# Kernel tuning notes

Measured on AMD Instinct MI355X. Metric: run time of the kernel, lower is better.

## Reference

```python
import jax, jax.numpy as jnp
import numpy as np

B, Q, K, D, H = 8, 200, 16384, 256, 8
ALIGN_K, CROSS_K, FF = 96, 1024, 1024
DH = D // H

def _l2norm(x):
    n = jnp.linalg.norm(x, axis=-1, keepdims=True)
    return x / jnp.maximum(n, 1e-6)

def _layernorm(x, g, b):
    mu = jnp.mean(x, axis=-1, keepdims=True)
    v = jnp.var(x, axis=-1, keepdims=True)
    return (x - mu) / jnp.sqrt(v + 1e-5) * g + b

def _mha(xq, xk, xv, in_w, in_b, out_w, out_b, bias=None):
    # torch nn.MultiheadAttention (batch_first, eval mode)
    wq, wk, wv = jnp.split(in_w, 3, axis=0)
    bq, bk, bv = jnp.split(in_b, 3, axis=0)
    def heads(x, w, bb):
        y = x @ w.T + bb
        return y.reshape(x.shape[0], x.shape[1], H, DH).transpose(0, 2, 1, 3)
    qh, kh, vh = heads(xq, wq, bq), heads(xk, wk, bk), heads(xv, wv, bv)
    s = jnp.einsum('bhqd,bhkd->bhqk', qh, kh) / (DH ** 0.5)
    if bias is not None:
        s = s + bias
    a = jax.nn.softmax(s, axis=-1)
    o = jnp.einsum('bhqk,bhkd->bhqd', a, vh).transpose(0, 2, 1, 3).reshape(xq.shape[0], xq.shape[1], D)
    return o @ out_w.T + out_b

def setup_inputs():
    key = jax.random.key(0)
    ks = jax.random.split(key, 40)
    r = lambda i, sh, s=1.0: jax.random.normal(ks[i], sh, jnp.float32) * s
    W = 0.02
    return dict(
        q=r(0, (B, Q, D)), q_pos=r(1, (B, Q, D)), memory=r(2, (B, K, D)),
        cross_attn_bias=r(3, (B, Q, K), 0.1),
        align_wq=r(4, (D, D), W), align_wm=r(5, (D, D), W),
        gate_w1=r(6, (D, 2 * D), W), gate_b1=jnp.zeros((D,), jnp.float32),
        gate_w2=r(7, (D, D), W), gate_b2=jnp.zeros((D,), jnp.float32),
        cross_wq=r(8, (D, D), W), cross_wm=r(9, (D, D), W),
        sa_in_w=r(10, (3 * D, D), W), sa_in_b=jnp.zeros((3 * D,), jnp.float32),
        sa_out_w=r(11, (D, D), W), sa_out_b=jnp.zeros((D,), jnp.float32),
        ca_in_w=r(12, (3 * D, D), W), ca_in_b=jnp.zeros((3 * D,), jnp.float32),
        ca_out_w=r(13, (D, D), W), ca_out_b=jnp.zeros((D,), jnp.float32),
        ffn_w1=r(14, (FF, D), W), ffn_b1=jnp.zeros((FF,), jnp.float32),
        ffn_w2=r(15, (D, FF), W), ffn_b2=jnp.zeros((D,), jnp.float32),
        n1_g=jnp.ones((D,), jnp.float32), n1_b=jnp.zeros((D,), jnp.float32),
        n2_g=jnp.ones((D,), jnp.float32), n2_b=jnp.zeros((D,), jnp.float32),
        n3_g=jnp.ones((D,), jnp.float32), n3_b=jnp.zeros((D,), jnp.float32))

def reference(q, q_pos, memory, cross_attn_bias, align_wq, align_wm, gate_w1, gate_b1,
              gate_w2, gate_b2, cross_wq, cross_wm, sa_in_w, sa_in_b, sa_out_w, sa_out_b,
              ca_in_w, ca_in_b, ca_out_w, ca_out_b, ffn_w1, ffn_b1, ffn_w2, ffn_b2,
              n1_g, n1_b, n2_g, n2_b, n3_g, n3_b):
    # --- query-memory align: proj+normalize+sim+topk+gather+softmax+weighted-sum ---
    qn = _l2norm(q @ align_wq.T)
    mn = _l2norm(memory @ align_wm.T)
    sim = jnp.einsum('bqd,bkd->bqk', qn, mn)            # [B,Q,K]
    vals, idx = jax.lax.top_k(sim, ALIGN_K)             # [B,Q,ALIGN_K]
    selected = jax.vmap(lambda m, i: m[i])(memory, idx) # [B,Q,ALIGN_K,D]
    w = jax.nn.softmax(vals, axis=-1)
    aligned = jnp.einsum('bqk,bqkd->bqd', w, selected)
    h = jax.nn.gelu(jnp.concatenate([q, aligned], axis=-1) @ gate_w1.T + gate_b1, approximate=False)
    gate = jax.nn.sigmoid(h @ gate_w2.T + gate_b2)
    qx = q + gate * aligned
    # --- self attention ---
    qk = qx + q_pos
    q2 = _mha(qk, qk, qx, sa_in_w, sa_in_b, sa_out_w, sa_out_b)
    qx = _layernorm(qx + q2, n1_g, n1_b)
    # --- cross-memory sparsify (topk over K) ---
    qn2 = _l2norm(qx @ cross_wq.T)
    mn2 = _l2norm(memory @ cross_wm.T)
    sim2 = jnp.einsum('bqd,bkd->bqk', qn2, mn2)
    importance = sim2.max(axis=1)                       # [B,K]
    _, kidx = jax.lax.top_k(importance, CROSS_K)        # [B,CROSS_K]
    mem_sel = jax.vmap(lambda m, i: m[i])(memory, kidx) # [B,CROSS_K,D]
    bias_sel = jnp.take_along_axis(
        cross_attn_bias, jnp.broadcast_to(kidx[:, None, :], (B, Q, CROSS_K)), axis=2)
    bias4 = jnp.broadcast_to(bias_sel[:, None], (B, H, Q, CROSS_K))
    q2 = _mha(qx + q_pos, mem_sel, mem_sel, ca_in_w, ca_in_b, ca_out_w, ca_out_b, bias4)
    qx = _layernorm(qx + q2, n2_g, n2_b)
    # --- FFN ---
    f = jax.nn.gelu(qx @ ffn_w1.T + ffn_b1, approximate=False) @ ffn_w2.T + ffn_b2
    return _layernorm(qx + f, n3_g, n3_b)
```

## Files before the change

### kernel.cpp

```cpp
#include <hip/hip_runtime.h>
#include <hip/hip_bf16.h>
#include <math.h>

#define B_ 8
#define Q_ 200
#define K_ 16384
#define D_ 256
#define H_ 8
#define DH_ 32
#define ALIGNK_ 96
#define CROSSK_ 1024
#define FF_ 1024
#define BQ_ (B_*Q_)
#define BK_ (B_*K_)

typedef unsigned short u16;
typedef short bf16x8 __attribute__((ext_vector_type(8)));
typedef float f32x4 __attribute__((ext_vector_type(4)));

__device__ __forceinline__ float b2f(u16 u){ return __uint_as_float(((unsigned)u)<<16); }
__device__ __forceinline__ u16 f2b(float f){
  unsigned x = __float_as_uint(f);
  unsigned r = x + 0x7FFFu + ((x>>16)&1u);
  return (u16)(r>>16);
}
__device__ __forceinline__ unsigned p2u(float lo, float hi){
  return (unsigned)f2b(lo) | ((unsigned)f2b(hi)<<16);
}
__device__ __forceinline__ uint4 pk8(float4 a, float4 b){
  return make_uint4(p2u(a.x,a.y), p2u(a.z,a.w), p2u(b.x,b.y), p2u(b.z,b.w));
}
__device__ __forceinline__ unsigned fkey(float f){ unsigned b=__float_as_uint(f); return (b&0x80000000u)? ~b : (b|0x80000000u); }
__device__ __forceinline__ float funkey(unsigned k){ unsigned b=(k&0x80000000u)? (k^0x80000000u) : ~k; return __uint_as_float(b); }
__device__ __forceinline__ float gelu_f(float x){ return 0.5f*x*(1.0f+erff(x*0.70710678118654752f)); }
__device__ __forceinline__ float sigmoid_f(float x){ return 1.0f/(1.0f+__expf(-x)); }

struct GArgs {
  const void* A; const void* B; const float* bias;
  float* Cf; u16* Cb; unsigned* amax;
  const int* gather;
  long lda, ldb, ldc;
  long sA, sB, sC, sAmax, sGather;
  int M, N, K, act;
};

template<int AF32, int BF32>
__global__ __launch_bounds__(256) void gemm_bt(GArgs g)
{
  const int tid = threadIdx.x;
  const int bz = blockIdx.z;
  const int m0 = blockIdx.y*64, n0 = blockIdx.x*64;
  const int lane = tid & 63, wave = tid >> 6;
  const int wr = wave >> 1, wc = wave & 1;
  __shared__ __align__(16) u16 As[64][72];
  __shared__ __align__(16) u16 Bs[64][72];
  f32x4 acc[2][2] = {};

  const int lrow = tid>>2;
  const int lk = (tid&3)*16;
  int ar = m0 + lrow; if (ar > g.M-1) ar = g.M-1;
  if (g.gather) ar = g.gather[(long)bz*g.sGather + ar];
  int br = n0 + lrow; if (br > g.N-1) br = g.N-1;
  long aoff = (long)bz*g.sA + (long)ar*g.lda + lk;
  long boff = (long)bz*g.sB + (long)br*g.ldb + lk;

  const int nk = g.K >> 6;
  for (int kt=0; kt<nk; ++kt){
    uint4 wa0, wa1, wb0, wb1;
    if (AF32){
      const float* p = (const float*)g.A + aoff;
      float4 f0 = *(const float4*)(p+0);
      float4 f1 = *(const float4*)(p+4);
      float4 f2v= *(const float4*)(p+8);
      float4 f3 = *(const float4*)(p+12);
      wa0 = pk8(f0,f1); wa1 = pk8(f2v,f3);
    } else {
      const u16* p = (const u16*)g.A + aoff;
      wa0 = *(const uint4*)p; wa1 = *(const uint4*)(p+8);
    }
    if (BF32){
      const float* p = (const float*)g.B + boff;
      float4 f0 = *(const float4*)(p+0);
      float4 f1 = *(const float4*)(p+4);
      float4 f2v= *(const float4*)(p+8);
      float4 f3 = *(const float4*)(p+12);
      wb0 = pk8(f0,f1); wb1 = pk8(f2v,f3);
    } else {
      const u16* p = (const u16*)g.B + boff;
      wb0 = *(const uint4*)p; wb1 = *(const uint4*)(p+8);
    }
    aoff += 64; boff += 64;
    __syncthreads();
    *(uint4*)&As[lrow][lk]   = wa0; *(uint4*)&As[lrow][lk+8] = wa1;
    *(uint4*)&Bs[lrow][lk]   = wb0; *(uint4*)&Bs[lrow][lk+8] = wb1;
    __syncthreads();
    #pragma unroll
    for (int kk=0; kk<2; ++kk){
      const int ko = kk*32 + (lane>>4)*8;
      bf16x8 af0 = *(const bf16x8*)&As[wr*32      + (lane&15)][ko];
      bf16x8 af1 = *(const bf16x8*)&As[wr*32 + 16 + (lane&15)][ko];
      bf16x8 bf0 = *(const bf16x8*)&Bs[wc*32      + (lane&15)][ko];
      bf16x8 bf1 = *(const bf16x8*)&Bs[wc*32 + 16 + (lane&15)][ko];
      acc[0][0] = __builtin_amdgcn_mfma_f32_16x16x32_bf16(af0, bf0, acc[0][0], 0,0,0);
      acc[0][1] = __builtin_amdgcn_mfma_f32_16x16x32_bf16(af0, bf1, acc[0][1], 0,0,0);
      acc[1][0] = __builtin_amdgcn_mfma_f32_16x16x32_bf16(af1, bf0, acc[1][0], 0,0,0);
      acc[1][1] = __builtin_amdgcn_mfma_f32_16x16x32_bf16(af1, bf1, acc[1][1], 0,0,0);
    }
  }

  if (g.amax){
    #pragma unroll
    for (int j=0;j<2;j++){
      float mx = -3.0e38f;
      #pragma unroll
      for (int i=0;i<2;i++)
        #pragma unroll
        for (int r=0;r<4;r++) mx = fmaxf(mx, acc[i][j][r]);
      mx = fmaxf(mx, __shfl_xor(mx, 16));
      mx = fmaxf(mx, __shfl_xor(mx, 32));
      if ((lane>>4)==0){
        int n = n0 + wc*32 + j*16 + (lane&15);
        if (n < g.N) atomicMax(&g.amax[(long)bz*g.sAmax + n], fkey(mx));
      }
    }
    return;
  }

  #pragma unroll
  for (int i=0;i<2;i++)
  #pragma unroll
  for (int j=0;j<2;j++)
  #pragma unroll
  for (int r=0;r<4;r++){
    int m = m0 + wr*32 + i*16 + (lane>>4)*4 + r;
    int n = n0 + wc*32 + j*16 + (lane&15);
    if (m < g.M && n < g.N){
      float v = acc[i][j][r];
      if (g.bias) v += g.bias[n];
      if (g.act==1) v = gelu_f(v);
      else if (g.act==2) v = sigmoid_f(v);
      long ci = (long)bz*g.sC + (long)m*g.ldc + n;
      if (g.Cf) g.Cf[ci] = v; else g.Cb[ci] = f2b(v);
    }
  }
}

template<int AF32>
__global__ __launch_bounds__(256) void proj_l2norm(
    const void* Ain, long lda, const float* W, u16* outp, int R)
{
  __shared__ __align__(16) u16 As[64][72];
  __shared__ __align__(16) u16 Bs[256][72];
  const int tid = threadIdx.x;
  const int m0 = blockIdx.x*64;
  const int lane = tid & 63, wave = tid >> 6;
  f32x4 acc[16] = {};

  const int lrow = tid>>2, lk = (tid&3)*16;
  int ar = m0 + lrow; if (ar > R-1) ar = R-1;

  for (int kt=0; kt<4; ++kt){
    uint4 wa0, wa1;
    if (AF32){
      const float* p = (const float*)Ain + (long)ar*lda + kt*64 + lk;
      wa0 = pk8(*(const float4*)(p+0), *(const float4*)(p+4));
      wa1 = pk8(*(const float4*)(p+8), *(const float4*)(p+12));
    } else {
      const u16* p = (const u16*)Ain + (long)ar*lda + kt*64 + lk;
      wa0 = *(const uint4*)p; wa1 = *(const uint4*)(p+8);
    }
    uint4 wb[8];
    {
      const float* wp = W + (long)tid*256 + kt*64;
      #pragma unroll
      for (int i=0;i<8;i++)
        wb[i] = pk8(*(const float4*)(wp + i*8), *(const float4*)(wp + i*8 + 4));
    }
    __syncthreads();
    *(uint4*)&As[lrow][lk] = wa0; *(uint4*)&As[lrow][lk+8] = wa1;
    #pragma unroll
    for (int i=0;i<8;i++) *(uint4*)&Bs[tid][i*8] = wb[i];
    __syncthreads();
    #pragma unroll
    for (int kk=0; kk<2; ++kk){
      const int ko = kk*32 + (lane>>4)*8;
      bf16x8 af = *(const bf16x8*)&As[wave*16 + (lane&15)][ko];
      #pragma unroll
      for (int jj=0; jj<16; jj++){
        bf16x8 bfr = *(const bf16x8*)&Bs[jj*16 + (lane&15)][ko];
        acc[jj] = __builtin_amdgcn_mfma_f32_16x16x32_bf16(af, bfr, acc[jj], 0,0,0);
      }
    }
  }

  #pragma unroll
  for (int r=0;r<4;r++){
    float ssq = 0.f;
    #pragma unroll
    for (int jj=0;jj<16;jj++) ssq += acc[jj][r]*acc[jj][r];
    ssq += __shfl_xor(ssq,1); ssq += __shfl_xor(ssq,2);
    ssq += __shfl_xor(ssq,4); ssq += __shfl_xor(ssq,8);
    float inv = 1.0f/fmaxf(sqrtf(ssq), 1e-6f);
    int row = m0 + wave*16 + (lane>>4)*4 + r;
    if (row < R){
      u16* op = outp + (long)row*256 + (lane&15);
      #pragma unroll
      for (int jj=0;jj<16;jj++) op[jj*16] = f2b(acc[jj][r]*inv);
    }
  }
}

__global__ __launch_bounds__(256) void topk_kernel(const float* inF, const unsigned* inK,
    long in_stride, int RANK, float* out_val, int* out_idx)
{
  __shared__ int red[2][4];
  __shared__ int redt[4];
  __shared__ int poss;
  int row = blockIdx.x, tid = threadIdx.x;
  unsigned kr[64];
  if (inF){
    const float4* p = (const float4*)(inF + (long)row*in_stride);
    #pragma unroll
    for (int jj=0;jj<16;jj++){
      float4 v = p[tid + jj*256];
      kr[jj*4+0]=fkey(v.x); kr[jj*4+1]=fkey(v.y); kr[jj*4+2]=fkey(v.z); kr[jj*4+3]=fkey(v.w);
    }
  } else {
    const uint4* p = (const uint4*)(inK + (long)row*in_stride);
    #pragma unroll
    for (int jj=0;jj<16;jj++){
      uint4 v = p[tid + jj*256];
      kr[jj*4+0]=v.x; kr[jj*4+1]=v.y; kr[jj*4+2]=v.z; kr[jj*4+3]=v.w;
    }
  }
  if (tid==0) poss = 0;

  unsigned u = 0; bool exact = false; int pp = 0;
  for (int bit=31; bit>=0; --bit){
    unsigned cand = u | (1u<<bit);
    int c = 0;
    #pragma unroll
    for (int j=0;j<64;j++) c += (kr[j] >= cand) ? 1 : 0;
    #pragma unroll
    for (int off=32; off; off>>=1) c += __shfl_down(c, off);
    if ((tid&63)==0) red[pp][tid>>6] = c;
    __syncthreads();
    c = red[pp][0]+red[pp][1]+red[pp][2]+red[pp][3];
    pp ^= 1;
    if (c >= RANK){
      u = cand;
      if (c == RANK){ exact = true; break; }
    }
  }

  int t = 0;
  if (!exact){
    int cgt = 0;
    #pragma unroll
    for (int j=0;j<64;j++) cgt += (kr[j] > u) ? 1 : 0;
    #pragma unroll
    for (int off=32; off; off>>=1) cgt += __shfl_down(cgt, off);
    __syncthreads();
    if ((tid&63)==0) redt[tid>>6] = cgt;
    __syncthreads();
    cgt = redt[0]+redt[1]+redt[2]+redt[3];
    int Req = RANK - cgt;
    for (int bit=13; bit>=0; --bit){
      int cand = t | (1<<bit);
      int c = 0;
      #pragma unroll
      for (int j=0;j<64;j++){
        int e = (tid<<2) + (j&3) + ((j>>2)<<10);
        c += (kr[j]==u && e < cand) ? 1 : 0;
      }
      #pragma unroll
      for (int off=32; off; off>>=1) c += __shfl_down(c, off);
      __syncthreads();
      if ((tid&63)==0) redt[tid>>6] = c;
      __syncthreads();
      c = redt[0]+redt[1]+redt[2]+redt[3];
      if (c < Req) t = cand;
    }
  }
  __syncthreads();
  #pragma unroll
  for (int j=0;j<64;j++){
    int e = (tid<<2) + (j&3) + ((j>>2)<<10);
    unsigned kk = kr[j];
    bool win = exact ? (kk >= u) : (kk > u || (kk == u && e <= t));
    if (win){
      int p2 = atomicAdd(&poss, 1);
      out_val[(long)row*RANK + p2] = funkey(kk);
      out_idx[(long)row*RANK + p2] = e;
    }
  }
}

__global__ __launch_bounds__(256) void align_combine(const float* vals, const int* idx,
    const float* memory, float* alignedv)
{
  __shared__ float w[96];
  __shared__ int id[96];
  __shared__ float reds[2];
  int row = blockIdx.x, tid = threadIdx.x;
  int b = row / 200;
  if (tid < 96){ w[tid] = vals[(long)row*96 + tid]; id[tid] = idx[(long)row*96 + tid]; }
  __syncthreads();
  if (tid < 64){
    float a = w[tid];
    float bb2 = (tid < 32) ? w[64+tid] : -3e38f;
    float m = fmaxf(a, bb2);
    #pragma unroll
    for (int off=32; off; off>>=1) m = fmaxf(m, __shfl_xor(m, off));
    if (tid==0) reds[0] = m;
  }
  __syncthreads();
  float m = reds[0];
  if (tid < 96) w[tid] = __expf(w[tid]-m);
  __syncthreads();
  if (tid < 64){
    float a = w[tid] + ((tid<32)? w[64+tid] : 0.f);
    #pragma unroll
    for (int off=32; off; off>>=1) a += __shfl_xor(a, off);
    if (tid==0) reds[1] = a;
  }
  __syncthreads();
  float invs = 1.0f/reds[1];
  float acc = 0.f;
  const float* mb = memory + (long)b*K_*D_;
  for (int k=0;k<96;k++) acc += w[k] * mb[(long)id[k]*D_ + tid];
  alignedv[(long)row*256 + tid] = acc*invs;
}

__global__ void make_cat(const float* q, const float* alignedv, u16* cat)
{
  int row = blockIdx.x, tid = threadIdx.x;
  long i = (long)row*256 + tid;
  cat[(long)row*512 + tid]       = f2b(q[i]);
  cat[(long)row*512 + 256 + tid] = f2b(alignedv[i]);
}

__global__ void combine_gate(const float* q, const float* q_pos, const float* alignedv,
    const float* gate, float* qx, u16* qx_b, u16* qk_b)
{
  int row = blockIdx.x, tid = threadIdx.x;
  long i = (long)row*256 + tid;
  float v = q[i] + gate[i]*alignedv[i];
  qx[i] = v;
  qx_b[i] = f2b(v);
  qk_b[i] = f2b(v + q_pos[i]);
}

__global__ __launch_bounds__(256) void add_ln(const float* x, const float* y,
    const float* g, const float* bb, const float* q_pos,
    float* out_f, u16* out_b, u16* out_pos_b)
{
  __shared__ float red[8];
  int row = blockIdx.x, tid = threadIdx.x;
  long i = (long)row*256 + tid;
  float t = fminf(fmaxf(x[i] + y[i], -1e6f), 1e6f);
  float s1 = t, s2 = t*t;
  #pragma unroll
  for (int off=32; off; off>>=1){ s1 += __shfl_down(s1,off); s2 += __shfl_down(s2,off); }
  if ((tid&63)==0){ red[(tid>>6)*2] = s1; red[(tid>>6)*2+1] = s2; }
  __syncthreads();
  s1 = red[0]+red[2]+red[4]+red[6];
  s2 = red[1]+red[3]+red[5]+red[7];
  float mu = s1 * (1.0f/256.0f);
  float var = fmaxf(s2 * (1.0f/256.0f) - mu*mu, 0.f);
  float rstd = rsqrtf(var + 1e-5f);
  float v = (t-mu)*rstd*g[tid] + bb[tid];
  if (out_f) out_f[i] = v;
  if (out_b) out_b[i] = f2b(v);
  if (out_pos_b) out_pos_b[i] = f2b(v + q_pos[i]);
}

__global__ void fill_u32(unsigned* p, unsigned val, int n)
{ int i = blockIdx.x*256 + threadIdx.x; if (i<n) p[i] = val; }

__global__ __launch_bounds__(256) void bias_gather(const float* cbias, const int* kidx,
    float* biasT)
{
  int b = blockIdx.y;
  int j = blockIdx.x*8 + (threadIdx.x>>5);
  int q = threadIdx.x & 31;
  int kid = kidx[b*CROSSK_ + j];
  const float* src = cbias + (long)b*Q_*K_ + kid;
  float* dst = biasT + ((long)b*CROSSK_ + j)*200;
  for (int qq=q; qq<200; qq+=32) dst[qq] = src[(long)qq*K_];
}

__global__ __launch_bounds__(256) void attn_kernel(
    const u16* Qb, int q_stride,
    const u16* KVb, int kv_stride, int k_off, int v_off, int Lk,
    const float* biasT,
    int nsplit, int chunk,
    float* opart, float* mlpart, float scale)
{
  __shared__ float Ks[64][36];
  __shared__ float Vs[64][36];
  const int b = blockIdx.z, h = blockIdx.y;
  const int split = blockIdx.x % nsplit;
  const int q0 = (blockIdx.x / nsplit) * 64;
  const int tid = threadIdx.x;
  const int cg = tid & 3, r = tid >> 2;
  const int kbeg = split*chunk;
  int kend = kbeg + chunk; if (kend > Lk) kend = Lk;

  int qr = q0 + r; if (qr > 199) qr = 199;
  float qreg[32];
  {
    const u16* qp = Qb + (long)(b*200+qr)*q_stride + h*32;
    #pragma unroll
    for (int w=0; w<4; w++){
      uint4 u = *(const uint4*)(qp + w*8);
      qreg[w*8+0]=b2f((u16)(u.x&0xffffu))*scale; qreg[w*8+1]=b2f((u16)(u.x>>16))*scale;
      qreg[w*8+2]=b2f((u16)(u.y&0xffffu))*scale; qreg[w*8+3]=b2f((u16)(u.y>>16))*scale;
      qreg[w*8+4]=b2f((u16)(u.z&0xffffu))*scale; qreg[w*8+5]=b2f((u16)(u.z>>16))*scale;
      qreg[w*8+6]=b2f((u16)(u.w&0xffffu))*scale; qreg[w*8+7]=b2f((u16)(u.w>>16))*scale;
    }
  }
  const float* bT = biasT ? biasT + ((long)b*CROSSK_)*200 + qr : nullptr;

  float o32[32];
  #pragma unroll
  for (int i=0;i<32;i++) o32[i]=0.f;
  float mrun = -3e38f, lrun = 0.f;

  const int srow = tid>>2, sc8 = (tid&3)*8;
  for (int j0=kbeg; j0<kend; j0+=64){
    int kr = j0 + srow; if (kr > kend-1) kr = kend-1;
    const long base = (long)(b*Lk + kr)*kv_stride;
    uint4 ku = *(const uint4*)(KVb + base + k_off + sc8);
    uint4 vu = *(const uint4*)(KVb + base + v_off + sc8);
    __syncthreads();
    {
      float4 f0, f1;
      f0.x=b2f((u16)(ku.x&0xffffu)); f0.y=b2f((u16)(ku.x>>16)); f0.z=b2f((u16)(ku.y&0xffffu)); f0.w=b2f((u16)(ku.y>>16));
      f1.x=b2f((u16)(ku.z&0xffffu)); f1.y=b2f((u16)(ku.z>>16)); f1.z=b2f((u16)(ku.w&0xffffu)); f1.w=b2f((u16)(ku.w>>16));
      *(float4*)&Ks[srow][sc8] = f0; *(float4*)&Ks[srow][sc8+4] = f1;
      f0.x=b2f((u16)(vu.x&0xffffu)); f0.y=b2f((u16)(vu.x>>16)); f0.z=b2f((u16)(vu.y&0xffffu)); f0.w=b2f((u16)(vu.y>>16));
      f1.x=b2f((u16)(vu.z&0xffffu)); f1.y=b2f((u16)(vu.z>>16)); f1.z=b2f((u16)(vu.w&0xffffu)); f1.w=b2f((u16)(vu.w>>16));
      *(float4*)&Vs[srow][sc8] = f0; *(float4*)&Vs[srow][sc8+4] = f1;
    }
    __syncthreads();

    float sv[16];
    float mloc = -3e38f;
    #pragma unroll
    for (int jj=0;jj<16;jj++){
      const int c = cg + jj*4;
      const float4* kp = (const float4*)&Ks[c][0];
      float a = 0.f;
      #pragma unroll
      for (int dq=0;dq<8;dq++){
        float4 kv = kp[dq];
        a += qreg[dq*4+0]*kv.x + qreg[dq*4+1]*kv.y + qreg[dq*4+2]*kv.z + qreg[dq*4+3]*kv.w;
      }
      if (biasT) a += bT[(long)(j0 + c)*200];
      if (j0 + c >= kend) a = -3e38f;
      sv[jj] = a; mloc = fmaxf(mloc, a);
    }
    mloc = fmaxf(mloc, __shfl_xor(mloc,1));
    mloc = fmaxf(mloc, __shfl_xor(mloc,2));
    const float mnew = fmaxf(mrun, mloc);
    const float alpha = __expf(mrun - mnew);
    float lloc = 0.f;
    #pragma unroll
    for (int jj=0;jj<16;jj++){
      float p = (j0 + cg + jj*4 >= kend) ? 0.f : __expf(sv[jj]-mnew);
      sv[jj] = p; lloc += p;
    }
    lloc += __shfl_xor(lloc,1);
    lloc += __shfl_xor(lloc,2);
    lrun = lrun*alpha + lloc;
    #pragma unroll
    for (int i=0;i<32;i++) o32[i] *= alpha;
    #pragma unroll
    for (int jj=0;jj<16;jj++){
      const int c = cg + jj*4;
      const float p = sv[jj];
      const float4* vp = (const float4*)&Vs[c][0];
      #pragma unroll
      for (int dq=0;dq<8;dq++){
        float4 v = vp[dq];
        o32[dq*4+0] += p*v.x; o32[dq*4+1] += p*v.y; o32[dq*4+2] += p*v.z; o32[dq*4+3] += p*v.w;
      }
    }
    mrun = mnew;
  }

  #pragma unroll
  for (int d=0;d<32;d++){
    float v = o32[d];
    v += __shfl_xor(v,1);
    v += __shfl_xor(v,2);
    o32[d] = v;
  }
  if (q0 + r < 200){
    const long pbase = (((long)(b*H_+h)*nsplit + split)*200) + (q0 + r);
    float* op = opart + pbase*32;
    #pragma unroll
    for (int i=0;i<8;i++) op[cg*8+i] = o32[cg*8+i];
    if (cg==0){ mlpart[pbase*2] = mrun; mlpart[pbase*2+1] = lrun; }
  }
}

__global__ __launch_bounds__(256) void attn_combine(const float* opart, const float* mlpart,
    int nsplit, u16* outp)
{
  int row = blockIdx.x;
  int b = row/200, qi = row%200;
  int tid = threadIdx.x;
  int h = tid>>5, d = tid&31;
  const long base = ((long)(b*H_+h)*nsplit)*200 + qi;
  float M = -3e38f;
  for (int s=0;s<nsplit;s++) M = fmaxf(M, mlpart[(base + (long)s*200)*2]);
  float L = 0.f, acc = 0.f;
  for (int s=0;s<nsplit;s++){
    const long ix = base + (long)s*200;
    float w = __expf(mlpart[ix*2] - M);
    L   += mlpart[ix*2+1]*w;
    acc += opart[ix*32 + d]*w;
  }
  outp[(long)row*256 + h*32 + d] = f2b(acc / fmaxf(L, 1e-30f));
}

extern "C" void kernel_launch(void* const* d_in, const int* in_sizes, int n_in,
                              void* d_out, int out_size, void* d_ws, size_t ws_size,
                              hipStream_t stream)
{
  const float* q        = (const float*)d_in[0];
  const float* q_pos    = (const float*)d_in[1];
  const float* memory   = (const float*)d_in[2];
  const float* cbias    = (const float*)d_in[3];
  const float* align_wq = (const float*)d_in[4];
  const float* align_wm = (const float*)d_in[5];
  const float* gate_w1  = (const float*)d_in[6];
  const float* gate_b1  = (const float*)d_in[7];
  const float* gate_w2  = (const float*)d_in[8];
  const float* gate_b2  = (const float*)d_in[9];
  const float* cross_wq = (const float*)d_in[10];
  const float* cross_wm = (const float*)d_in[11];
  const float* sa_in_w  = (const float*)d_in[12];
  const float* sa_in_b  = (const float*)d_in[13];
  const float* sa_out_w = (const float*)d_in[14];
  const float* sa_out_b = (const float*)d_in[15];
  const float* ca_in_w  = (const float*)d_in[16];
  const float* ca_in_b  = (const float*)d_in[17];
  const float* ca_out_w = (const float*)d_in[18];
  const float* ca_out_b = (const float*)d_in[19];
  const float* ffn_w1   = (const float*)d_in[20];
  const float* ffn_b1   = (const float*)d_in[21];
  const float* ffn_w2   = (const float*)d_in[22];
  const float* ffn_b2   = (const float*)d_in[23];
  const float* n1_g = (const float*)d_in[24];
  const float* n1_b = (const float*)d_in[25];
  const float* n2_g = (const float*)d_in[26];
  const float* n2_b = (const float*)d_in[27];
  const float* n3_g = (const float*)d_in[28];
  const float* n3_b = (const float*)d_in[29];
  float* out = (float*)d_out;

  char* wsb = (char*)d_ws;
  size_t off = 0;
  auto alloc = [&](size_t bytes)->char*{
    char* p = wsb + off; off = (off + bytes + 255) & ~(size_t)255; return p;
  };
  const int NSPLIT = 4;
  u16*    qn_bf   = (u16*)   alloc((size_t)BQ_*D_*2);
  float*  vals96  = (float*) alloc((size_t)BQ_*96*4);
  int*    idx96   = (int*)   alloc((size_t)BQ_*96*4);
  float*  alignedv= (float*) alloc((size_t)BQ_*D_*4);
  u16*    cat_bf  = (u16*)   alloc((size_t)BQ_*512*2);
  u16*    h_bf    = (u16*)   alloc((size_t)BQ_*D_*2);
  float*  gatebuf = (float*) alloc((size_t)BQ_*D_*4);
  float*  qx      = (float*) alloc((size_t)BQ_*D_*4);
  u16*    qx_bf   = (u16*)   alloc((size_t)BQ_*D_*2);
  u16*    qk_bf   = (u16*)   alloc((size_t)BQ_*D_*2);
  u16*    qpos2_bf= (u16*)   alloc((size_t)BQ_*D_*2);
  u16*    qkv_bf  = (u16*)   alloc((size_t)BQ_*768*2);
  u16*    attO_bf = (u16*)   alloc((size_t)BQ_*D_*2);
  float*  q2      = (float*) alloc((size_t)BQ_*D_*4);
  unsigned* imp   = (unsigned*)alloc((size_t)B_*K_*4);
  int*    kidx    = (int*)   alloc((size_t)B_*CROSSK_*4);
  u16*    cq_bf   = (u16*)   alloc((size_t)BQ_*D_*2);
  u16*    f1_bf   = (u16*)   alloc((size_t)BQ_*FF_*2);
  float*  f2buf   = (float*) alloc((size_t)BQ_*D_*4);
  float*  opart   = (float*) alloc((size_t)B_*H_*NSPLIT*200*32*4);
  float*  mlpart  = (float*) alloc((size_t)B_*H_*NSPLIT*200*2*4);
  float*  biasT   = (float*) alloc((size_t)B_*CROSSK_*200*4);

  const size_t kv_bytes   = (size_t)B_*CROSSK_*512*2;
  const size_t mn_full    = (size_t)BK_*D_*2;
  const size_t mn_small   = (size_t)K_*D_*2;
  const size_t sim_full   = (size_t)BQ_*K_*4;
  size_t remain = (ws_size > off) ? ws_size - off : 0;
  bool fullws = remain >= mn_full + sim_full + (1u<<20);
  size_t mn_bytes = fullws ? mn_full : (mn_small > kv_bytes ? mn_small : kv_bytes);
  int simRows;
  if (fullws) simRows = BQ_;
  else {
    size_t left = (remain > mn_bytes + (1u<<18)) ? remain - mn_bytes - (1u<<18) : 0;
    long r = (long)(left / ((size_t)K_*4));
    simRows = (int)(r < 8 ? 8 : (r > Q_ ? Q_ : r));
  }
  u16*   mn_bf  = (u16*)  alloc(mn_bytes);
  u16*   kvbuf  = (u16*)  mn_bf;
  float* simbuf = (float*)alloc((size_t)simRows*K_*4);

  auto gemm = [&](int af32, int bf32,
                  const void* A, long lda, long sA,
                  const void* Bm, long ldb, long sB,
                  int M, int N, int Kd,
                  const float* bias, int act,
                  float* Cf, u16* Cb, long ldc, long sC,
                  unsigned* amax, long sAmax,
                  const int* gather, long sGather, int Z){
    GArgs ga;
    ga.A=A; ga.B=Bm; ga.bias=bias; ga.Cf=Cf; ga.Cb=Cb; ga.amax=amax; ga.gather=gather;
    ga.lda=lda; ga.ldb=ldb; ga.ldc=ldc; ga.sA=sA; ga.sB=sB; ga.sC=sC;
    ga.sAmax=sAmax; ga.sGather=sGather;
    ga.M=M; ga.N=N; ga.K=Kd; ga.act=act;
    dim3 grid(N/64, (M+63)/64, Z);
    if (af32 && bf32)      gemm_bt<1,1><<<grid, 256, 0, stream>>>(ga);
    else if (af32)         gemm_bt<1,0><<<grid, 256, 0, stream>>>(ga);
    else if (bf32)         gemm_bt<0,1><<<grid, 256, 0, stream>>>(ga);
    else                   gemm_bt<0,0><<<grid, 256, 0, stream>>>(ga);
  };
  const float ascale = 0.17677669529663687f;

  proj_l2norm<1><<<BQ_/64,256,0,stream>>>(q, 256, align_wq, qn_bf, BQ_);
  if (fullws){
    proj_l2norm<1><<<BK_/64,256,0,stream>>>(memory, 256, align_wm, mn_bf, BK_);
    gemm(0,0, qn_bf,256,(long)200*256, mn_bf,256,(long)K_*256, 200,K_,256,
         nullptr,0, simbuf,nullptr,K_,(long)200*K_, nullptr,0, nullptr,0, B_);
    topk_kernel<<<BQ_,256,0,stream>>>(simbuf, nullptr, K_, 96, vals96, idx96);
  } else {
    for (int b=0;b<B_;b++){
      proj_l2norm<1><<<K_/64,256,0,stream>>>(memory + (size_t)b*K_*256, 256, align_wm, mn_bf, K_);
      for (int q0=0; q0<Q_; q0+=simRows){
        int rows = (Q_ - q0 < simRows) ? (Q_ - q0) : simRows;
        gemm(0,0, qn_bf + ((size_t)b*200+q0)*256,256,0, mn_bf,256,0, rows,K_,256,
             nullptr,0, simbuf,nullptr,K_,0, nullptr,0, nullptr,0, 1);
        topk_kernel<<<rows,256,0,stream>>>(simbuf, nullptr, K_, 96,
             vals96 + ((size_t)b*200+q0)*96, idx96 + ((size_t)b*200+q0)*96);
      }
    }
  }
  align_combine<<<BQ_,256,0,stream>>>(vals96, idx96, memory, alignedv);

  make_cat<<<BQ_,256,0,stream>>>(q, alignedv, cat_bf);
  gemm(0,1, cat_bf,512,0, gate_w1,512,0, BQ_,256,512, gate_b1,1, nullptr,h_bf,256,0, nullptr,0, nullptr,0, 1);
  gemm(0,1, h_bf,256,0, gate_w2,256,0, BQ_,256,256, gate_b2,2, gatebuf,nullptr,256,0, nullptr,0, nullptr,0, 1);
  combine_gate<<<BQ_,256,0,stream>>>(q, q_pos, alignedv, gatebuf, qx, qx_bf, qk_bf);

  gemm(0,1, qk_bf,256,0, sa_in_w,256,0, BQ_,512,256, sa_in_b,0, nullptr,qkv_bf,768,0, nullptr,0, nullptr,0, 1);
  gemm(0,1, qx_bf,256,0, sa_in_w+512*256,256,0, BQ_,256,256, sa_in_b+512,0, nullptr,qkv_bf+512,768,0, nullptr,0, nullptr,0, 1);
  attn_kernel<<<dim3(4*NSPLIT,H_,B_),256,0,stream>>>(qkv_bf,768, qkv_bf,768,256,512,200,
      nullptr, NSPLIT,64, opart,mlpart, ascale);
  attn_combine<<<BQ_,256,0,stream>>>(opart, mlpart, NSPLIT, attO_bf);
  gemm(0,1, attO_bf,256,0, sa_out_w,256,0, BQ_,256,256, sa_out_b,0, q2,nullptr,256,0, nullptr,0, nullptr,0, 1);
  add_ln<<<BQ_,256,0,stream>>>(qx, q2, n1_g, n1_b, q_pos, qx, qx_bf, qpos2_bf);

  proj_l2norm<0><<<BQ_/64,256,0,stream>>>(qx_bf, 256, cross_wq, qn_bf, BQ_);
  fill_u32<<<(B_*K_+255)/256,256,0,stream>>>(imp, 0u, B_*K_);
  if (fullws){
    proj_l2norm<1><<<BK_/64,256,0,stream>>>(memory, 256, cross_wm, mn_bf, BK_);
    gemm(0,0, qn_bf,256,(long)200*256, mn_bf,256,(long)K_*256, 200,K_,256,
         nullptr,0, nullptr,nullptr,0,0, imp,(long)K_, nullptr,0, B_);
  } else {
    for (int b=0;b<B_;b++){
      proj_l2norm<1><<<K_/64,256,0,stream>>>(memory + (size_t)b*K_*256, 256, cross_wm, mn_bf, K_);
      gemm(0,0, qn_bf + (size_t)b*200*256,256,0, mn_bf,256,0, 200,K_,256,
           nullptr,0, nullptr,nullptr,0,0, imp + (size_t)b*K_,(long)K_, nullptr,0, 1);
    }
  }
  topk_kernel<<<B_,256,0,stream>>>(nullptr, imp, K_, CROSSK_, vals96 , kidx);

  bias_gather<<<dim3(CROSSK_/8, B_),256,0,stream>>>(cbias, kidx, biasT);
  gemm(1,1, memory,256,(long)K_*256, ca_in_w+256*256,256,0, CROSSK_,512,256,
       ca_in_b+256,0, nullptr,kvbuf,512,(long)CROSSK_*512, nullptr,0, kidx,(long)CROSSK_, B_);
  gemm(0,1, qpos2_bf,256,0, ca_in_w,256,0, BQ_,256,256, ca_in_b,0, nullptr,cq_bf,256,0, nullptr,0, nullptr,0, 1);
  attn_kernel<<<dim3(4*NSPLIT,H_,B_),256,0,stream>>>(cq_bf,256, kvbuf,512,0,256,CROSSK_,
      biasT, NSPLIT,256, opart,mlpart, ascale);
  attn_combine<<<BQ_,256,0,stream>>>(opart, mlpart, NSPLIT, attO_bf);
  gemm(0,1, attO_bf,256,0, ca_out_w,256,0, BQ_,256,256, ca_out_b,0, q2,nullptr,256,0, nullptr,0, nullptr,0, 1);
  add_ln<<<BQ_,256,0,stream>>>(qx, q2, n2_g, n2_b, nullptr, qx, qx_bf, nullptr);

  gemm(0,1, qx_bf,256,0, ffn_w1,256,0, BQ_,FF_,256, ffn_b1,1, nullptr,f1_bf,FF_,0, nullptr,0, nullptr,0, 1);
  gemm(0,1, f1_bf,FF_,0, ffn_w2,FF_,0, BQ_,256,FF_, ffn_b2,0, f2buf,nullptr,256,0, nullptr,0, nullptr,0, 1);
  add_ln<<<BQ_,256,0,stream>>>(qx, f2buf, n3_g, n3_b, nullptr, out, nullptr, nullptr);

  (void)in_sizes; (void)n_in; (void)out_size;
}
```

Measured before the change: 994.3 us.

## Pre-convert projection weights to bf16 and shrink proj_l2norm shared tile

Adds a small kernel that converts the four projection weight matrices to bf16 once per call. proj_l2norm then reads bf16 weights in four 64-column chunks through a 64x72 shared tile instead of converting fp32 weights per block into a 256-row tile. This removes repeated fp32 weight loads and packing in the large memory-projection launches and cuts shared memory per block, which may raise occupancy. The cost is more barriers per k-step and four extra small kernel launches.

```diff
diff --git a/kernel.cpp b/kernel.cpp
--- a/kernel.cpp
+++ b/kernel.cpp
@@ -145,16 +145,25 @@
   }
 }
 
+__global__ void w2b_kernel(const float* w, u16* wb, int n)
+{
+  int i = (blockIdx.x*256 + threadIdx.x)*8;
+  if (i < n){
+    float4 a = *(const float4*)(w+i), b = *(const float4*)(w+i+4);
+    *(uint4*)(wb+i) = pk8(a,b);
+  }
+}
+
 template<int AF32>
 __global__ __launch_bounds__(256) void proj_l2norm(
-    const void* Ain, long lda, const float* W, u16* outp, int R)
+    const void* Ain, long lda, const u16* Wb, u16* outp, int R)
 {
   __shared__ __align__(16) u16 As[64][72];
-  __shared__ __align__(16) u16 Bs[256][72];
+  __shared__ __align__(16) u16 Bs[64][72];
   const int tid = threadIdx.x;
   const int m0 = blockIdx.x*64;
   const int lane = tid & 63, wave = tid >> 6;
-  f32x4 acc[16] = {};
+  f32x4 acc[4][4] = {};
 
   const int lrow = tid>>2, lk = (tid&3)*16;
   int ar = m0 + lrow; if (ar > R-1) ar = R-1;
@@ -169,26 +178,24 @@
       const u16* p = (const u16*)Ain + (long)ar*lda + kt*64 + lk;
       wa0 = *(const uint4*)p; wa1 = *(const uint4*)(p+8);
     }
-    uint4 wb[8];
-    {
-      const float* wp = W + (long)tid*256 + kt*64;
+    #pragma unroll
+    for (int nc=0; nc<4; ++nc){
+      const u16* wp = Wb + (long)(nc*64 + lrow)*256 + kt*64 + lk;
+      uint4 wb0 = *(const uint4*)wp;
+      uint4 wb1 = *(const uint4*)(wp+8);
+      __syncthreads();
+      if (nc==0){ *(uint4*)&As[lrow][lk] = wa0; *(uint4*)&As[lrow][lk+8] = wa1; }
+      *(uint4*)&Bs[lrow][lk] = wb0; *(uint4*)&Bs[lrow][lk+8] = wb1;
+      __syncthreads();
       #pragma unroll
-      for (int i=0;i<8;i++)
-        wb[i] = pk8(*(const float4*)(wp + i*8), *(const float4*)(wp + i*8 + 4));
-    }
-    __syncthreads();
-    *(uint4*)&As[lrow][lk] = wa0; *(uint4*)&As[lrow][lk+8] = wa1;
-    #pragma unroll
-    for (int i=0;i<8;i++) *(uint4*)&Bs[tid][i*8] = wb[i];
-    __syncthreads();
-    #pragma unroll
-    for (int kk=0; kk<2; ++kk){
-      const int ko = kk*32 + (lane>>4)*8;
-      bf16x8 af = *(const bf16x8*)&As[wave*16 + (lane&15)][ko];
-      #pragma unroll
-      for (int jj=0; jj<16; jj++){
-        bf16x8 bfr = *(const bf16x8*)&Bs[jj*16 + (lane&15)][ko];
-        acc[jj] = __builtin_amdgcn_mfma_f32_16x16x32_bf16(af, bfr, acc[jj], 0,0,0);
+      for (int kk=0; kk<2; ++kk){
+        const int ko = kk*32 + (lane>>4)*8;
+        bf16x8 af = *(const bf16x8*)&As[wave*16 + (lane&15)][ko];
+        #pragma unroll
+        for (int j=0; j<4; j++){
+          bf16x8 bfr = *(const bf16x8*)&Bs[j*16 + (lane&15)][ko];
+          acc[nc][j] = __builtin_amdgcn_mfma_f32_16x16x32_bf16(af, bfr, acc[nc][j], 0,0,0);
+        }
       }
     }
   }
@@ -197,7 +204,9 @@
   for (int r=0;r<4;r++){
     float ssq = 0.f;
     #pragma unroll
-    for (int jj=0;jj<16;jj++) ssq += acc[jj][r]*acc[jj][r];
+    for (int nc=0;nc<4;nc++)
+      #pragma unroll
+      for (int j=0;j<4;j++) ssq += acc[nc][j][r]*acc[nc][j][r];
     ssq += __shfl_xor(ssq,1); ssq += __shfl_xor(ssq,2);
     ssq += __shfl_xor(ssq,4); ssq += __shfl_xor(ssq,8);
     float inv = 1.0f/fmaxf(sqrtf(ssq), 1e-6f);
@@ -205,7 +214,9 @@
     if (row < R){
       u16* op = outp + (long)row*256 + (lane&15);
       #pragma unroll
-      for (int jj=0;jj<16;jj++) op[jj*16] = f2b(acc[jj][r]*inv);
+      for (int nc=0;nc<4;nc++)
+        #pragma unroll
+        for (int j=0;j<4;j++) op[nc*64 + j*16] = f2b(acc[nc][j][r]*inv);
     }
   }
 }
@@ -590,6 +601,10 @@
   float*  opart   = (float*) alloc((size_t)B_*H_*NSPLIT*200*32*4);
   float*  mlpart  = (float*) alloc((size_t)B_*H_*NSPLIT*200*2*4);
   float*  biasT   = (float*) alloc((size_t)B_*CROSSK_*200*4);
+  u16*    wb_alwq = (u16*)   alloc((size_t)D_*D_*2);
+  u16*    wb_alwm = (u16*)   alloc((size_t)D_*D_*2);
+  u16*    wb_crwq = (u16*)   alloc((size_t)D_*D_*2);
+  u16*    wb_crwm = (u16*)   alloc((size_t)D_*D_*2);
 
   const size_t kv_bytes   = (size_t)B_*CROSSK_*512*2;
   const size_t mn_full    = (size_t)BK_*D_*2;
@@ -630,15 +645,20 @@
   };
   const float ascale = 0.17677669529663687f;
 
-  proj_l2norm<1><<<BQ_/64,256,0,stream>>>(q, 256, align_wq, qn_bf, BQ_);
+  w2b_kernel<<<32,256,0,stream>>>(align_wq, wb_alwq, D_*D_);
+  w2b_kernel<<<32,256,0,stream>>>(align_wm, wb_alwm, D_*D_);
+  w2b_kernel<<<32,256,0,stream>>>(cross_wq, wb_crwq, D_*D_);
+  w2b_kernel<<<32,256,0,stream>>>(cross_wm, wb_crwm, D_*D_);
+
+  proj_l2norm<1><<<BQ_/64,256,0,stream>>>(q, 256, wb_alwq, qn_bf, BQ_);
   if (fullws){
-    proj_l2norm<1><<<BK_/64,256,0,stream>>>(memory, 256, align_wm, mn_bf, BK_);
+    proj_l2norm<1><<<BK_/64,256,0,stream>>>(memory, 256, wb_alwm, mn_bf, BK_);
     gemm(0,0, qn_bf,256,(long)200*256, mn_bf,256,(long)K_*256, 200,K_,256,
          nullptr,0, simbuf,nullptr,K_,(long)200*K_, nullptr,0, nullptr,0, B_);
     topk_kernel<<<BQ_,256,0,stream>>>(simbuf, nullptr, K_, 96, vals96, idx96);
   } else {
     for (int b=0;b<B_;b++){
-      proj_l2norm<1><<<K_/64,256,0,stream>>>(memory + (size_t)b*K_*256, 256, align_wm, mn_bf, K_);
+      proj_l2norm<1><<<K_/64,256,0,stream>>>(memory + (size_t)b*K_*256, 256, wb_alwm, mn_bf, K_);
       for (int q0=0; q0<Q_; q0+=simRows){
         int rows = (Q_ - q0 < simRows) ? (Q_ - q0) : simRows;
         gemm(0,0, qn_bf + ((size_t)b*200+q0)*256,256,0, mn_bf,256,0, rows,K_,256,
@@ -663,15 +683,15 @@
   gemm(0,1, attO_bf,256,0, sa_out_w,256,0, BQ_,256,256, sa_out_b,0, q2,nullptr,256,0, nullptr,0, nullptr,0, 1);
   add_ln<<<BQ_,256,0,stream>>>(qx, q2, n1_g, n1_b, q_pos, qx, qx_bf, qpos2_bf);
 
-  proj_l2norm<0><<<BQ_/64,256,0,stream>>>(qx_bf, 256, cross_wq, qn_bf, BQ_);
+  proj_l2norm<0><<<BQ_/64,256,0,stream>>>(qx_bf, 256, wb_crwq, qn_bf, BQ_);
   fill_u32<<<(B_*K_+255)/256,256,0,stream>>>(imp, 0u, B_*K_);
   if (fullws){
-    proj_l2norm<1><<<BK_/64,256,0,stream>>>(memory, 256, cross_wm, mn_bf, BK_);
+    proj_l2norm<1><<<BK_/64,256,0,stream>>>(memory, 256, wb_crwm, mn_bf, BK_);
     gemm(0,0, qn_bf,256,(long)200*256, mn_bf,256,(long)K_*256, 200,K_,256,
          nullptr,0, nullptr,nullptr,0,0, imp,(long)K_, nullptr,0, B_);
   } else {
     for (int b=0;b<B_;b++){
-      proj_l2norm<1><<<K_/64,256,0,stream>>>(memory + (size_t)b*K_*256, 256, cross_wm, mn_bf, K_);
+      proj_l2norm<1><<<K_/64,256,0,stream>>>(memory + (size_t)b*K_*256, 256, wb_crwm, mn_bf, K_);
       gemm(0,0, qn_bf + (size_t)b*200*256,256,0, mn_bf,256,0, 200,K_,256,
            nullptr,0, nullptr,nullptr,0,0, imp + (size_t)b*K_,(long)K_, nullptr,0, 1);
     }
```

Result: faster. 916.0 us (-7.9%).
